# Optimization experiments

Hardware: AMD Instinct MI355X
Metric: run time of the kernel (lower is better)

The kernel has to match this reference:

```python
import jax, jax.numpy as jnp
import numpy as np
import math

DIM = 4096      # hidden size
NH = 32         # query heads
NKV = 8         # kv heads (GQA)
HD = 128        # head dim
SW = 4096       # sliding window / cache length
B = 8           # batch (decode)
START_POS = 2047
PAD_LEN = min(((START_POS + 1 + 31) // 32) * 32, SW)  # nearest_32 -> 2048
ROPE_THETA = 10000.0


def _rotation_matrix(pos, dhead, theta=ROPE_THETA):
    # freqs_to_rotation_matrix: block-diagonal 2x2 rotations, applied as q @ R
    freqs = 1.0 / (theta ** (np.arange(0, dhead, 2, dtype=np.float64) / dhead))
    ang = pos * freqs
    cos, sin = np.cos(ang), np.sin(ang)
    rot = np.zeros((dhead, dhead), dtype=np.float32)
    ev = np.arange(0, dhead, 2)
    od = ev + 1
    rot[ev, ev] = cos
    rot[od, od] = cos
    rot[ev, od] = -sin
    rot[od, ev] = sin
    return rot


def setup_inputs() -> dict:
    key = jax.random.key(0)
    ks = jax.random.split(key, 8)
    s = 0.02
    x = jax.random.normal(ks[0], (1, 1, B, DIM), jnp.float32)
    wq = jax.random.normal(ks[1], (DIM, NH * HD), jnp.float32) * s
    wk = jax.random.normal(ks[2], (DIM, NKV * HD), jnp.float32) * s
    wv = jax.random.normal(ks[3], (DIM, NKV * HD), jnp.float32) * s
    wo = jax.random.normal(ks[4], (NH * HD, DIM), jnp.float32) * s
    # true RoPE rotation matrix for the current position, same for all batch rows
    rot = jnp.asarray(_rotation_matrix(START_POS, HD))
    rot_mat = jnp.broadcast_to(rot, (1, B, HD, HD))
    # KV cache: valid history in [0, START_POS), rest is garbage that gets masked
    cache_k = jax.random.normal(ks[5], (B, NKV, SW, HD), jnp.float32) * s
    cache_v = jax.random.normal(ks[6], (B, NKV, SW, HD), jnp.float32) * s
    # additive mask: 0 for positions <= start_pos, finfo.min after
    neg = jnp.finfo(jnp.float32).min
    mask_row = jnp.where(jnp.arange(PAD_LEN) <= START_POS, 0.0, neg).astype(jnp.float32)
    attn_mask = jnp.broadcast_to(mask_row, (1, NH, B, PAD_LEN))
    return {
        "x": x, "wq": wq, "wk": wk, "wv": wv, "wo": wo,
        "rot_mat": rot_mat, "cache_k": cache_k, "cache_v": cache_v,
        "attn_mask": attn_mask, "start_pos": START_POS,
    }


def reference(x, wq, wk, wv, wo, rot_mat, cache_k, cache_v, attn_mask, start_pos):
    scale = 1.0 / math.sqrt(HD)
    xb = x[0, 0]                                  # (B, DIM)
    # fused QKV projection
    q = (xb @ wq).reshape(B, NH, HD)              # (B, NH, HD)
    k = (xb @ wk).reshape(B, NKV, HD)             # (B, NKV, HD)
    v = (xb @ wv).reshape(B, NKV, HD)             # (B, NKV, HD)
    # RoPE via explicit rotation-matrix matmul (per batch row)
    rm = rot_mat[0]                               # (B, HD, HD)
    q = jnp.einsum('bhd,bde->bhe', q, rm)
    k = jnp.einsum('bgd,bde->bge', k, rm)
    # update_cache at position `oldest` (= start_pos since start_pos < sliding_window)
    ck = cache_k.at[:, :, start_pos].set(k)
    cv = cache_v.at[:, :, start_pos].set(v)
    keys = ck[:, :, :PAD_LEN]                     # (B, NKV, L, HD)
    vals = cv[:, :, :PAD_LEN]                     # (B, NKV, L, HD)
    # grouped attention: NH query heads share NKV kv heads
    qg = q.reshape(B, NKV, NH // NKV, HD)
    scores = jnp.einsum('bgqd,bgld->bgql', qg, keys) * scale
    # attn_mask: (1, NH, B, L) -> (B, NKV, NH//NKV, L)
    mask = attn_mask[0].transpose(1, 0, 2).reshape(B, NKV, NH // NKV, PAD_LEN)
    probs = jax.nn.softmax(scores + mask, axis=-1)
    out = jnp.einsum('bgql,bgld->bgqd', probs, vals).reshape(B, NH * HD)
    dense = out @ wo                              # (B, DIM)
    return dense.reshape(1, 1, B, DIM)
```

## Files before the change

### kernel.cpp

```cpp
#include <hip/hip_runtime.h>
#include <math.h>

#define DIM 4096
#define NH 32
#define NKV 8
#define HD 128
#define B_ 8
#define SW 4096
#define PAD_LEN 2048
#define GQ 4
#define QKV_COLS (DIM + 2 * NKV * HD)
#define KSQ 64
#define KCQ (DIM / KSQ)
#define KSO 64
#define KCO (DIM / KSO)
#define LCHUNK 256
#define NLCHUNK (PAD_LEN / LCHUNK)
#define SCALE 0.08838834764831845f

#define OFF_QKVP   0
#define OFF_Q      (OFF_QKVP + KSQ * B_ * QKV_COLS)
#define OFF_K      (OFF_Q + B_ * DIM)
#define OFF_V      (OFF_K + B_ * NKV * HD)
#define OFF_AP     (OFF_V + B_ * NKV * HD)
#define OFF_AO     (OFF_AP + B_ * NKV * NLCHUNK * GQ * (HD + 2))
#define OFF_OP     (OFF_AO + B_ * DIM)

__global__ void qkv_partial(const float* __restrict__ x,
                            const float* __restrict__ wq,
                            const float* __restrict__ wk,
                            const float* __restrict__ wv,
                            float* __restrict__ part) {
    __shared__ float xs[B_][KCQ];
    const int tid = threadIdx.x;
    const int k0  = blockIdx.y * KCQ;

    {
        int idx = tid * 2;
        int r   = idx >> 6;
        int kk  = idx & (KCQ - 1);
        float2 xv = *(const float2*)(x + r * DIM + k0 + kk);
        xs[r][kk]     = xv.x;
        xs[r][kk + 1] = xv.y;
    }
    __syncthreads();

    const int bx = blockIdx.x;
    const float* W;
    int ldw, cbase;
    if (bx < 8)       { W = wq; ldw = NH * HD;  cbase = bx * 512; }
    else if (bx < 10) { W = wk; ldw = NKV * HD; cbase = (bx - 8) * 512; }
    else              { W = wv; ldw = NKV * HD; cbase = (bx - 10) * 512; }
    const int c = cbase + tid * 2;

    float2 acc[B_];
    #pragma unroll
    for (int r = 0; r < B_; ++r) { acc[r].x = 0.f; acc[r].y = 0.f; }

    const float* wp = W + (size_t)k0 * ldw + c;
    #pragma unroll 8
    for (int kk = 0; kk < KCQ; ++kk) {
        float2 w = *(const float2*)(wp + (size_t)kk * ldw);
        #pragma unroll
        for (int r = 0; r < B_; ++r) {
            float xv = xs[r][kk];
            acc[r].x = fmaf(xv, w.x, acc[r].x);
            acc[r].y = fmaf(xv, w.y, acc[r].y);
        }
    }
    const int colg = bx * 512 + tid * 2;
    #pragma unroll
    for (int r = 0; r < B_; ++r)
        *(float2*)(part + ((size_t)(blockIdx.y * B_ + r)) * QKV_COLS + colg) = acc[r];
}

__global__ void qkv_reduce_rope(const float* __restrict__ part,
                                const float* __restrict__ rot,
                                float* __restrict__ qb,
                                float* __restrict__ kb,
                                float* __restrict__ vb) {
    const int tid  = threadIdx.x;
    const int col2 = blockIdx.x * 256 + tid;
    const int col  = col2 * 2;
    const int r    = blockIdx.y;

    float2 v; v.x = 0.f; v.y = 0.f;
    #pragma unroll 8
    for (int s = 0; s < KSQ; ++s) {
        float2 p = *(const float2*)(part + ((size_t)(s * B_ + r)) * QKV_COLS + col);
        v.x += p.x; v.y += p.y;
    }

    if (col < DIM + NKV * HD) {
        int hd = col & (HD - 1);
        const float* rm = rot + (size_t)r * HD * HD;
        float c  = rm[hd * HD + hd];
        float sn = rm[(hd + 1) * HD + hd];
        float2 o;
        o.x = v.x * c + v.y * sn;
        o.y = v.y * c - v.x * sn;
        if (col < DIM) *(float2*)(qb + r * DIM + col) = o;
        else           *(float2*)(kb + r * NKV * HD + (col - DIM)) = o;
    } else {
        *(float2*)(vb + r * NKV * HD + (col - DIM - NKV * HD)) = v;
    }
}

__global__ void attn_partial(const float* __restrict__ qb,
                             const float* __restrict__ knew,
                             const float* __restrict__ vnew,
                             const float* __restrict__ cache_k,
                             const float* __restrict__ cache_v,
                             const float* __restrict__ mask,
                             const int* __restrict__ start_pos_p,
                             float* __restrict__ part) {
    const int bg = blockIdx.x;
    const int b  = bg >> 3;
    const int g  = bg & 7;
    const int chunk = blockIdx.y;
    const int l0 = chunk * LCHUNK;
    const int tid = threadIdx.x;
    const int sp = start_pos_p[0];

    __shared__ float q_lds[GQ][HD];
    __shared__ float p_lds[GQ][LCHUNK];
    __shared__ float crossm[4][GQ];
    __shared__ float crosss[4][GQ];

    for (int i = tid; i < GQ * HD; i += 256) {
        int qh = i >> 7;
        int d  = i & (HD - 1);
        q_lds[qh][d] = qb[b * DIM + (g * GQ + qh) * HD + d];
    }
    __syncthreads();

    const int l = l0 + tid;
    const float* krow = (l == sp) ? (knew + (b * NKV + g) * HD)
                                  : (cache_k + (((size_t)(b * NKV + g)) * SW + l) * HD);
    float s[GQ] = {0.f, 0.f, 0.f, 0.f};
    const float4* k4 = (const float4*)krow;
    #pragma unroll 8
    for (int j = 0; j < HD / 4; ++j) {
        float4 kv = k4[j];
        #pragma unroll
        for (int qh = 0; qh < GQ; ++qh) {
            s[qh] += kv.x * q_lds[qh][4*j]   + kv.y * q_lds[qh][4*j+1]
                   + kv.z * q_lds[qh][4*j+2] + kv.w * q_lds[qh][4*j+3];
        }
    }
    float sv[GQ];
    #pragma unroll
    for (int qh = 0; qh < GQ; ++qh)
        sv[qh] = s[qh] * SCALE
               + mask[(((size_t)(g * GQ + qh)) * B_ + b) * PAD_LEN + l];

    const int wave = tid >> 6;
    const int lane = tid & 63;
    float wm[GQ];
    #pragma unroll
    for (int qh = 0; qh < GQ; ++qh) wm[qh] = sv[qh];
    #pragma unroll
    for (int off = 32; off > 0; off >>= 1)
        #pragma unroll
        for (int qh = 0; qh < GQ; ++qh)
            wm[qh] = fmaxf(wm[qh], __shfl_xor(wm[qh], off, 64));
    if (lane == 0)
        #pragma unroll
        for (int qh = 0; qh < GQ; ++qh) crossm[wave][qh] = wm[qh];
    __syncthreads();
    float m[GQ];
    #pragma unroll
    for (int qh = 0; qh < GQ; ++qh)
        m[qh] = fmaxf(fmaxf(crossm[0][qh], crossm[1][qh]),
                      fmaxf(crossm[2][qh], crossm[3][qh]));

    float wsum[GQ];
    #pragma unroll
    for (int qh = 0; qh < GQ; ++qh) {
        float p = __expf(sv[qh] - m[qh]);
        p_lds[qh][tid] = p;
        wsum[qh] = p;
    }
    #pragma unroll
    for (int off = 32; off > 0; off >>= 1)
        #pragma unroll
        for (int qh = 0; qh < GQ; ++qh)
            wsum[qh] += __shfl_xor(wsum[qh], off, 64);
    if (lane == 0)
        #pragma unroll
        for (int qh = 0; qh < GQ; ++qh) crosss[wave][qh] = wsum[qh];
    __syncthreads();
    float sum[GQ];
    #pragma unroll
    for (int qh = 0; qh < GQ; ++qh)
        sum[qh] = crosss[0][qh] + crosss[1][qh] + crosss[2][qh] + crosss[3][qh];

    const int qh = wave;
    const int d2 = lane * 2;
    float2 acc; acc.x = 0.f; acc.y = 0.f;
    const float* vbase = cache_v + (((size_t)(b * NKV + g)) * SW) * HD + d2;
    const float* vnewp = vnew + (b * NKV + g) * HD + d2;
    #pragma unroll 4
    for (int ll = 0; ll < LCHUNK; ++ll) {
        int lg = l0 + ll;
        const float* vp = (lg == sp) ? vnewp : (vbase + (size_t)lg * HD);
        float2 vv = *(const float2*)vp;
        float p = p_lds[qh][ll];
        acc.x = fmaf(p, vv.x, acc.x);
        acc.y = fmaf(p, vv.y, acc.y);
    }

    const size_t base = ((size_t)bg * NLCHUNK + chunk) * GQ;
    *(float2*)(part + (base + qh) * (HD + 2) + 2 + d2) = acc;
    if (tid < GQ) {
        part[(base + tid) * (HD + 2) + 0] = m[tid];
        part[(base + tid) * (HD + 2) + 1] = sum[tid];
    }
}

__global__ void attn_combine(const float* __restrict__ part,
                             float* __restrict__ attnout) {
    const int bg = blockIdx.x;
    const int b  = bg >> 3;
    const int g  = bg & 7;
    const int d  = threadIdx.x;

    for (int qh = 0; qh < GQ; ++qh) {
        float M = -3.4e38f;
        #pragma unroll
        for (int c = 0; c < NLCHUNK; ++c)
            M = fmaxf(M, part[(((size_t)bg * NLCHUNK + c) * GQ + qh) * (HD + 2)]);
        float denom = 0.f, o = 0.f;
        #pragma unroll
        for (int c = 0; c < NLCHUNK; ++c) {
            const float* p = part + (((size_t)bg * NLCHUNK + c) * GQ + qh) * (HD + 2);
            float w = __expf(p[0] - M);
            denom += w * p[1];
            o     += w * p[2 + d];
        }
        attnout[b * DIM + (g * GQ + qh) * HD + d] = o / denom;
    }
}

__global__ void oproj_partial(const float* __restrict__ xin,
                              const float* __restrict__ wo,
                              float* __restrict__ part) {
    __shared__ float xs[B_][KCO];
    const int tid = threadIdx.x;
    const int k0  = blockIdx.y * KCO;

    {
        int idx = tid * 2;
        int r   = idx >> 6;
        int kk  = idx & (KCO - 1);
        float2 xv = *(const float2*)(xin + r * DIM + k0 + kk);
        xs[r][kk]     = xv.x;
        xs[r][kk + 1] = xv.y;
    }
    __syncthreads();

    const int col = blockIdx.x * 512 + tid * 2;
    float2 acc[B_];
    #pragma unroll
    for (int r = 0; r < B_; ++r) { acc[r].x = 0.f; acc[r].y = 0.f; }

    const float* wp = wo + (size_t)k0 * DIM + col;
    #pragma unroll 8
    for (int kk = 0; kk < KCO; ++kk) {
        float2 w = *(const float2*)(wp + (size_t)kk * DIM);
        #pragma unroll
        for (int r = 0; r < B_; ++r) {
            float xv = xs[r][kk];
            acc[r].x = fmaf(xv, w.x, acc[r].x);
            acc[r].y = fmaf(xv, w.y, acc[r].y);
        }
    }
    #pragma unroll
    for (int r = 0; r < B_; ++r)
        *(float2*)(part + ((size_t)(blockIdx.y * B_ + r)) * DIM + col) = acc[r];
}

__global__ void oproj_reduce(const float* __restrict__ part,
                             float* __restrict__ out) {
    const int tid = threadIdx.x;
    const int col = (blockIdx.x * 256 + tid) * 2;
    const int r   = blockIdx.y;
    float2 v; v.x = 0.f; v.y = 0.f;
    #pragma unroll 8
    for (int s = 0; s < KSO; ++s) {
        float2 p = *(const float2*)(part + ((size_t)(s * B_ + r)) * DIM + col);
        v.x += p.x; v.y += p.y;
    }
    *(float2*)(out + r * DIM + col) = v;
}

extern "C" void kernel_launch(void* const* d_in, const int* in_sizes, int n_in,
                              void* d_out, int out_size, void* d_ws, size_t ws_size,
                              hipStream_t stream) {
    const float* x        = (const float*)d_in[0];
    const float* wq       = (const float*)d_in[1];
    const float* wk       = (const float*)d_in[2];
    const float* wv       = (const float*)d_in[3];
    const float* wo       = (const float*)d_in[4];
    const float* rot      = (const float*)d_in[5];
    const float* cache_k  = (const float*)d_in[6];
    const float* cache_v  = (const float*)d_in[7];
    const float* mask     = (const float*)d_in[8];
    const int*   start_pp = (const int*)d_in[9];
    float* ws  = (float*)d_ws;
    float* out = (float*)d_out;

    dim3 gA(QKV_COLS / 512, KSQ);
    qkv_partial<<<gA, 256, 0, stream>>>(x, wq, wk, wv, ws + OFF_QKVP);

    dim3 gB((QKV_COLS / 2) / 256, B_);
    qkv_reduce_rope<<<gB, 256, 0, stream>>>(ws + OFF_QKVP, rot,
                                            ws + OFF_Q, ws + OFF_K, ws + OFF_V);

    dim3 gC(B_ * NKV, NLCHUNK);
    attn_partial<<<gC, 256, 0, stream>>>(ws + OFF_Q, ws + OFF_K, ws + OFF_V,
                                         cache_k, cache_v, mask, start_pp,
                                         ws + OFF_AP);

    attn_combine<<<dim3(B_ * NKV), 128, 0, stream>>>(ws + OFF_AP, ws + OFF_AO);

    dim3 gD(DIM / 512, KSO);
    oproj_partial<<<gD, 256, 0, stream>>>(ws + OFF_AO, wo, ws + OFF_OP);

    dim3 gE((DIM / 2) / 256, B_);
    oproj_reduce<<<gE, 256, 0, stream>>>(ws + OFF_OP, out);
}
```

Measured before the change: 129.3 us.

## Rework GEMV split-K with float4 tiles and restage attention via LDS

The QKV and output-projection GEMVs move to float4 column tiles with twice as many K-splits, and their reduce kernels split the partial sum across four waves and combine through shared memory. Attention uses 64-position chunks: each block stages K rows in padded shared memory, computes one query head per wave with a wave-local softmax, and accumulates V for all four heads before a cross-wave reduction. The goal is wider loads and more parallelism across the memory-bound stages. The cost is larger partial buffers, more combine work, and more blocks to schedule.

```diff
diff --git a/kernel.cpp b/kernel.cpp
--- a/kernel.cpp
+++ b/kernel.cpp
@@ -10,11 +10,11 @@
 #define PAD_LEN 2048
 #define GQ 4
 #define QKV_COLS (DIM + 2 * NKV * HD)
-#define KSQ 64
+#define KSQ 128
 #define KCQ (DIM / KSQ)
-#define KSO 64
+#define KSO 128
 #define KCO (DIM / KSO)
-#define LCHUNK 256
+#define LCHUNK 64
 #define NLCHUNK (PAD_LEN / LCHUNK)
 #define SCALE 0.08838834764831845f
 
@@ -26,200 +26,213 @@
 #define OFF_AO     (OFF_AP + B_ * NKV * NLCHUNK * GQ * (HD + 2))
 #define OFF_OP     (OFF_AO + B_ * DIM)
 
-__global__ void qkv_partial(const float* __restrict__ x,
-                            const float* __restrict__ wq,
-                            const float* __restrict__ wk,
-                            const float* __restrict__ wv,
-                            float* __restrict__ part) {
+__global__ __launch_bounds__(256)
+void qkv_partial(const float* __restrict__ x,
+                 const float* __restrict__ wq,
+                 const float* __restrict__ wk,
+                 const float* __restrict__ wv,
+                 float* __restrict__ part) {
     __shared__ float xs[B_][KCQ];
     const int tid = threadIdx.x;
     const int k0  = blockIdx.y * KCQ;
 
-    {
-        int idx = tid * 2;
-        int r   = idx >> 6;
-        int kk  = idx & (KCQ - 1);
-        float2 xv = *(const float2*)(x + r * DIM + k0 + kk);
-        xs[r][kk]     = xv.x;
-        xs[r][kk + 1] = xv.y;
+    if (tid < 64) {
+        int r  = tid >> 3;
+        int kk = (tid & 7) * 4;
+        *(float4*)&xs[r][kk] = *(const float4*)(x + r * DIM + k0 + kk);
     }
     __syncthreads();
 
     const int bx = blockIdx.x;
     const float* W;
     int ldw, cbase;
-    if (bx < 8)       { W = wq; ldw = NH * HD;  cbase = bx * 512; }
-    else if (bx < 10) { W = wk; ldw = NKV * HD; cbase = (bx - 8) * 512; }
-    else              { W = wv; ldw = NKV * HD; cbase = (bx - 10) * 512; }
-    const int c = cbase + tid * 2;
-
-    float2 acc[B_];
-    #pragma unroll
-    for (int r = 0; r < B_; ++r) { acc[r].x = 0.f; acc[r].y = 0.f; }
+    if (bx < 4)       { W = wq; ldw = NH * HD;  cbase = bx * 1024; }
+    else if (bx == 4) { W = wk; ldw = NKV * HD; cbase = 0; }
+    else              { W = wv; ldw = NKV * HD; cbase = 0; }
+    const int c = cbase + tid * 4;
+
+    float4 acc[B_];
+    #pragma unroll
+    for (int r = 0; r < B_; ++r) { acc[r].x = acc[r].y = acc[r].z = acc[r].w = 0.f; }
 
     const float* wp = W + (size_t)k0 * ldw + c;
     #pragma unroll 8
     for (int kk = 0; kk < KCQ; ++kk) {
-        float2 w = *(const float2*)(wp + (size_t)kk * ldw);
+        float4 w = *(const float4*)(wp + (size_t)kk * ldw);
         #pragma unroll
         for (int r = 0; r < B_; ++r) {
             float xv = xs[r][kk];
             acc[r].x = fmaf(xv, w.x, acc[r].x);
             acc[r].y = fmaf(xv, w.y, acc[r].y);
-        }
-    }
-    const int colg = bx * 512 + tid * 2;
+            acc[r].z = fmaf(xv, w.z, acc[r].z);
+            acc[r].w = fmaf(xv, w.w, acc[r].w);
+        }
+    }
+    const int colg = bx * 1024 + tid * 4;
     #pragma unroll
     for (int r = 0; r < B_; ++r)
-        *(float2*)(part + ((size_t)(blockIdx.y * B_ + r)) * QKV_COLS + colg) = acc[r];
-}
-
-__global__ void qkv_reduce_rope(const float* __restrict__ part,
-                                const float* __restrict__ rot,
-                                float* __restrict__ qb,
-                                float* __restrict__ kb,
-                                float* __restrict__ vb) {
-    const int tid  = threadIdx.x;
-    const int col2 = blockIdx.x * 256 + tid;
-    const int col  = col2 * 2;
+        *(float4*)(part + ((size_t)(blockIdx.y * B_ + r)) * QKV_COLS + colg) = acc[r];
+}
+
+__global__ __launch_bounds__(256)
+void qkv_reduce_rope(const float* __restrict__ part,
+                     const float* __restrict__ rot,
+                     float* __restrict__ qb,
+                     float* __restrict__ kb,
+                     float* __restrict__ vb) {
+    __shared__ float4 red[4][64];
+    const int tid = threadIdx.x;
+    const int sg  = tid >> 6;
+    const int c4l = tid & 63;
+    const int col4 = blockIdx.x * 64 + c4l;
     const int r    = blockIdx.y;
 
-    float2 v; v.x = 0.f; v.y = 0.f;
-    #pragma unroll 8
-    for (int s = 0; s < KSQ; ++s) {
-        float2 p = *(const float2*)(part + ((size_t)(s * B_ + r)) * QKV_COLS + col);
-        v.x += p.x; v.y += p.y;
-    }
-
-    if (col < DIM + NKV * HD) {
-        int hd = col & (HD - 1);
-        const float* rm = rot + (size_t)r * HD * HD;
-        float c  = rm[hd * HD + hd];
-        float sn = rm[(hd + 1) * HD + hd];
-        float2 o;
-        o.x = v.x * c + v.y * sn;
-        o.y = v.y * c - v.x * sn;
-        if (col < DIM) *(float2*)(qb + r * DIM + col) = o;
-        else           *(float2*)(kb + r * NKV * HD + (col - DIM)) = o;
-    } else {
-        *(float2*)(vb + r * NKV * HD + (col - DIM - NKV * HD)) = v;
-    }
-}
-
-__global__ void attn_partial(const float* __restrict__ qb,
-                             const float* __restrict__ knew,
-                             const float* __restrict__ vnew,
-                             const float* __restrict__ cache_k,
-                             const float* __restrict__ cache_v,
-                             const float* __restrict__ mask,
-                             const int* __restrict__ start_pos_p,
-                             float* __restrict__ part) {
+    float4 v; v.x = v.y = v.z = v.w = 0.f;
+    const int s0 = sg * (KSQ / 4);
+    #pragma unroll 8
+    for (int s = s0; s < s0 + KSQ / 4; ++s) {
+        float4 p = *(const float4*)(part + ((size_t)(s * B_ + r)) * QKV_COLS + col4 * 4);
+        v.x += p.x; v.y += p.y; v.z += p.z; v.w += p.w;
+    }
+    red[sg][c4l] = v;
+    __syncthreads();
+
+    if (tid < 64) {
+        const int c4 = blockIdx.x * 64 + tid;
+        float4 a = red[0][tid], b2 = red[1][tid], c2 = red[2][tid], d2 = red[3][tid];
+        float4 vv;
+        vv.x = a.x + b2.x + c2.x + d2.x;
+        vv.y = a.y + b2.y + c2.y + d2.y;
+        vv.z = a.z + b2.z + c2.z + d2.z;
+        vv.w = a.w + b2.w + c2.w + d2.w;
+        const int col = c4 * 4;
+        if (col < DIM + NKV * HD) {
+            int hd = col & (HD - 1);
+            const float* rm = rot + (size_t)r * HD * HD;
+            float c0 = rm[hd * HD + hd];
+            float s0r = rm[(hd + 1) * HD + hd];
+            float c1 = rm[(hd + 2) * HD + hd + 2];
+            float s1r = rm[(hd + 3) * HD + hd + 2];
+            float4 o;
+            o.x = vv.x * c0 + vv.y * s0r;
+            o.y = vv.y * c0 - vv.x * s0r;
+            o.z = vv.z * c1 + vv.w * s1r;
+            o.w = vv.w * c1 - vv.z * s1r;
+            if (col < DIM) *(float4*)(qb + r * DIM + col) = o;
+            else           *(float4*)(kb + r * NKV * HD + (col - DIM)) = o;
+        } else {
+            *(float4*)(vb + r * NKV * HD + (col - DIM - NKV * HD)) = vv;
+        }
+    }
+}
+
+__global__ __launch_bounds__(256)
+void attn_partial(const float* __restrict__ qb,
+                  const float* __restrict__ knew,
+                  const float* __restrict__ vnew,
+                  const float* __restrict__ cache_k,
+                  const float* __restrict__ cache_v,
+                  const float* __restrict__ mask,
+                  const int* __restrict__ start_pos_p,
+                  float* __restrict__ part) {
     const int bg = blockIdx.x;
     const int b  = bg >> 3;
     const int g  = bg & 7;
     const int chunk = blockIdx.y;
     const int l0 = chunk * LCHUNK;
-    const int tid = threadIdx.x;
+    const int tid  = threadIdx.x;
+    const int lane = tid & 63;
+    const int wave = tid >> 6;
     const int sp = start_pos_p[0];
 
+    __shared__ float k_lds[LCHUNK][HD + 4];
     __shared__ float q_lds[GQ][HD];
     __shared__ float p_lds[GQ][LCHUNK];
-    __shared__ float crossm[4][GQ];
-    __shared__ float crosss[4][GQ];
-
-    for (int i = tid; i < GQ * HD; i += 256) {
-        int qh = i >> 7;
-        int d  = i & (HD - 1);
-        q_lds[qh][d] = qb[b * DIM + (g * GQ + qh) * HD + d];
-    }
-    __syncthreads();
-
-    const int l = l0 + tid;
-    const float* krow = (l == sp) ? (knew + (b * NKV + g) * HD)
-                                  : (cache_k + (((size_t)(b * NKV + g)) * SW + l) * HD);
-    float s[GQ] = {0.f, 0.f, 0.f, 0.f};
-    const float4* k4 = (const float4*)krow;
-    #pragma unroll 8
-    for (int j = 0; j < HD / 4; ++j) {
-        float4 kv = k4[j];
+    __shared__ float vred[4][GQ][HD];
+
+    if (tid < 128) {
+        int qh = tid >> 5;
+        int d4 = (tid & 31) * 4;
+        *(float4*)&q_lds[qh][d4] = *(const float4*)(qb + b * DIM + (g * GQ + qh) * HD + d4);
+    }
+    const float* kc = cache_k + ((size_t)(b * NKV + g)) * SW * HD;
+    const float* knp = knew + (b * NKV + g) * HD;
+    #pragma unroll
+    for (int i = 0; i < 8; ++i) {
+        int idx = i * 256 + tid;
+        int r   = idx >> 5;
+        int c4  = (idx & 31) * 4;
+        int lg  = l0 + r;
+        const float* src = (lg == sp) ? knp : (kc + (size_t)lg * HD);
+        *(float4*)&k_lds[r][c4] = *(const float4*)(src + c4);
+    }
+    __syncthreads();
+
+    const int qh = wave;
+    const int row = lane;
+    float s = 0.f;
+    #pragma unroll 8
+    for (int d = 0; d < HD; d += 4) {
+        float4 kv = *(const float4*)&k_lds[row][d];
+        float4 qv = *(const float4*)&q_lds[qh][d];
+        s += kv.x * qv.x + kv.y * qv.y + kv.z * qv.z + kv.w * qv.w;
+    }
+    const int l = l0 + row;
+    float sv = s * SCALE + mask[(((size_t)(g * GQ + qh)) * B_ + b) * PAD_LEN + l];
+
+    float m = sv;
+    #pragma unroll
+    for (int off = 32; off > 0; off >>= 1)
+        m = fmaxf(m, __shfl_xor(m, off, 64));
+    float p = __expf(sv - m);
+    float sum = p;
+    #pragma unroll
+    for (int off = 32; off > 0; off >>= 1)
+        sum += __shfl_xor(sum, off, 64);
+    p_lds[qh][row] = p;
+    __syncthreads();
+
+    const int d2 = lane * 2;
+    const float* vc  = cache_v + ((size_t)(b * NKV + g)) * SW * HD;
+    const float* vnp = vnew + (b * NKV + g) * HD;
+    float2 acc[GQ];
+    #pragma unroll
+    for (int q = 0; q < GQ; ++q) { acc[q].x = 0.f; acc[q].y = 0.f; }
+    #pragma unroll 4
+    for (int ll = 0; ll < LCHUNK / 4; ++ll) {
+        int r  = wave * (LCHUNK / 4) + ll;
+        int lg = l0 + r;
+        const float* vp = ((lg == sp) ? vnp : (vc + (size_t)lg * HD)) + d2;
+        float2 vv = *(const float2*)vp;
         #pragma unroll
-        for (int qh = 0; qh < GQ; ++qh) {
-            s[qh] += kv.x * q_lds[qh][4*j]   + kv.y * q_lds[qh][4*j+1]
-                   + kv.z * q_lds[qh][4*j+2] + kv.w * q_lds[qh][4*j+3];
-        }
-    }
-    float sv[GQ];
-    #pragma unroll
-    for (int qh = 0; qh < GQ; ++qh)
-        sv[qh] = s[qh] * SCALE
-               + mask[(((size_t)(g * GQ + qh)) * B_ + b) * PAD_LEN + l];
-
-    const int wave = tid >> 6;
-    const int lane = tid & 63;
-    float wm[GQ];
-    #pragma unroll
-    for (int qh = 0; qh < GQ; ++qh) wm[qh] = sv[qh];
-    #pragma unroll
-    for (int off = 32; off > 0; off >>= 1)
-        #pragma unroll
-        for (int qh = 0; qh < GQ; ++qh)
-            wm[qh] = fmaxf(wm[qh], __shfl_xor(wm[qh], off, 64));
-    if (lane == 0)
-        #pragma unroll
-        for (int qh = 0; qh < GQ; ++qh) crossm[wave][qh] = wm[qh];
-    __syncthreads();
-    float m[GQ];
-    #pragma unroll
-    for (int qh = 0; qh < GQ; ++qh)
-        m[qh] = fmaxf(fmaxf(crossm[0][qh], crossm[1][qh]),
-                      fmaxf(crossm[2][qh], crossm[3][qh]));
-
-    float wsum[GQ];
-    #pragma unroll
-    for (int qh = 0; qh < GQ; ++qh) {
-        float p = __expf(sv[qh] - m[qh]);
-        p_lds[qh][tid] = p;
-        wsum[qh] = p;
-    }
-    #pragma unroll
-    for (int off = 32; off > 0; off >>= 1)
-        #pragma unroll
-        for (int qh = 0; qh < GQ; ++qh)
-            wsum[qh] += __shfl_xor(wsum[qh], off, 64);
-    if (lane == 0)
-        #pragma unroll
-        for (int qh = 0; qh < GQ; ++qh) crosss[wave][qh] = wsum[qh];
-    __syncthreads();
-    float sum[GQ];
-    #pragma unroll
-    for (int qh = 0; qh < GQ; ++qh)
-        sum[qh] = crosss[0][qh] + crosss[1][qh] + crosss[2][qh] + crosss[3][qh];
-
-    const int qh = wave;
-    const int d2 = lane * 2;
-    float2 acc; acc.x = 0.f; acc.y = 0.f;
-    const float* vbase = cache_v + (((size_t)(b * NKV + g)) * SW) * HD + d2;
-    const float* vnewp = vnew + (b * NKV + g) * HD + d2;
-    #pragma unroll 4
-    for (int ll = 0; ll < LCHUNK; ++ll) {
-        int lg = l0 + ll;
-        const float* vp = (lg == sp) ? vnewp : (vbase + (size_t)lg * HD);
-        float2 vv = *(const float2*)vp;
-        float p = p_lds[qh][ll];
-        acc.x = fmaf(p, vv.x, acc.x);
-        acc.y = fmaf(p, vv.y, acc.y);
-    }
-
+        for (int q = 0; q < GQ; ++q) {
+            float pp = p_lds[q][r];
+            acc[q].x = fmaf(pp, vv.x, acc[q].x);
+            acc[q].y = fmaf(pp, vv.y, acc[q].y);
+        }
+    }
+    #pragma unroll
+    for (int q = 0; q < GQ; ++q)
+        *(float2*)&vred[wave][q][d2] = acc[q];
+    __syncthreads();
+
+    float2 o; o.x = 0.f; o.y = 0.f;
+    #pragma unroll
+    for (int w = 0; w < 4; ++w) {
+        float2 t = *(const float2*)&vred[w][qh][d2];
+        o.x += t.x; o.y += t.y;
+    }
     const size_t base = ((size_t)bg * NLCHUNK + chunk) * GQ;
-    *(float2*)(part + (base + qh) * (HD + 2) + 2 + d2) = acc;
-    if (tid < GQ) {
-        part[(base + tid) * (HD + 2) + 0] = m[tid];
-        part[(base + tid) * (HD + 2) + 1] = sum[tid];
-    }
-}
-
-__global__ void attn_combine(const float* __restrict__ part,
-                             float* __restrict__ attnout) {
+    *(float2*)(part + (base + qh) * (HD + 2) + 2 + d2) = o;
+    if (lane == 0) {
+        part[(base + qh) * (HD + 2) + 0] = m;
+        part[(base + qh) * (HD + 2) + 1] = sum;
+    }
+}
+
+__global__ __launch_bounds__(128)
+void attn_combine(const float* __restrict__ part,
+                  float* __restrict__ attnout) {
     const int bg = blockIdx.x;
     const int b  = bg >> 3;
     const int g  = bg & 7;
@@ -227,11 +240,11 @@
 
     for (int qh = 0; qh < GQ; ++qh) {
         float M = -3.4e38f;
-        #pragma unroll
+        #pragma unroll 8
         for (int c = 0; c < NLCHUNK; ++c)
             M = fmaxf(M, part[(((size_t)bg * NLCHUNK + c) * GQ + qh) * (HD + 2)]);
         float denom = 0.f, o = 0.f;
-        #pragma unroll
+        #pragma unroll 8
         for (int c = 0; c < NLCHUNK; ++c) {
             const float* p = part + (((size_t)bg * NLCHUNK + c) * GQ + qh) * (HD + 2);
             float w = __expf(p[0] - M);
@@ -242,56 +255,74 @@
     }
 }
 
-__global__ void oproj_partial(const float* __restrict__ xin,
-                              const float* __restrict__ wo,
-                              float* __restrict__ part) {
+__global__ __launch_bounds__(256)
+void oproj_partial(const float* __restrict__ xin,
+                   const float* __restrict__ wo,
+                   float* __restrict__ part) {
     __shared__ float xs[B_][KCO];
     const int tid = threadIdx.x;
     const int k0  = blockIdx.y * KCO;
 
-    {
-        int idx = tid * 2;
-        int r   = idx >> 6;
-        int kk  = idx & (KCO - 1);
-        float2 xv = *(const float2*)(xin + r * DIM + k0 + kk);
-        xs[r][kk]     = xv.x;
-        xs[r][kk + 1] = xv.y;
-    }
-    __syncthreads();
-
-    const int col = blockIdx.x * 512 + tid * 2;
-    float2 acc[B_];
-    #pragma unroll
-    for (int r = 0; r < B_; ++r) { acc[r].x = 0.f; acc[r].y = 0.f; }
+    if (tid < 64) {
+        int r  = tid >> 3;
+        int kk = (tid & 7) * 4;
+        *(float4*)&xs[r][kk] = *(const float4*)(xin + r * DIM + k0 + kk);
+    }
+    __syncthreads();
+
+    const int col = blockIdx.x * 1024 + tid * 4;
+    float4 acc[B_];
+    #pragma unroll
+    for (int r = 0; r < B_; ++r) { acc[r].x = acc[r].y = acc[r].z = acc[r].w = 0.f; }
 
     const float* wp = wo + (size_t)k0 * DIM + col;
     #pragma unroll 8
     for (int kk = 0; kk < KCO; ++kk) {
-        float2 w = *(const float2*)(wp + (size_t)kk * DIM);
+        float4 w = *(const float4*)(wp + (size_t)kk * DIM);
         #pragma unroll
         for (int r = 0; r < B_; ++r) {
             float xv = xs[r][kk];
             acc[r].x = fmaf(xv, w.x, acc[r].x);
             acc[r].y = fmaf(xv, w.y, acc[r].y);
+            acc[r].z = fmaf(xv, w.z, acc[r].z);
+            acc[r].w = fmaf(xv, w.w, acc[r].w);
         }
     }
     #pragma unroll
     for (int r = 0; r < B_; ++r)
-        *(float2*)(part + ((size_t)(blockIdx.y * B_ + r)) * DIM + col) = acc[r];
-}
-
-__global__ void oproj_reduce(const float* __restrict__ part,
-                             float* __restrict__ out) {
+        *(float4*)(part + ((size_t)(blockIdx.y * B_ + r)) * DIM + col) = acc[r];
+}
+
+__global__ __launch_bounds__(256)
+void oproj_reduce(const float* __restrict__ part,
+                  float* __restrict__ out) {
+    __shared__ float4 red[4][64];
     const int tid = threadIdx.x;
-    const int col = (blockIdx.x * 256 + tid) * 2;
-    const int r   = blockIdx.y;
-    float2 v; v.x = 0.f; v.y = 0.f;
-    #pragma unroll 8
-    for (int s = 0; s < KSO; ++s) {
-        float2 p = *(const float2*)(part + ((size_t)(s * B_ + r)) * DIM + col);
-        v.x += p.x; v.y += p.y;
-    }
-    *(float2*)(out + r * DIM + col) = v;
+    const int sg  = tid >> 6;
+    const int c4l = tid & 63;
+    const int col4 = blockIdx.x * 64 + c4l;
+    const int r    = blockIdx.y;
+
+    float4 v; v.x = v.y = v.z = v.w = 0.f;
+    const int s0 = sg * (KSO / 4);
+    #pragma unroll 8
+    for (int s = s0; s < s0 + KSO / 4; ++s) {
+        float4 p = *(const float4*)(part + ((size_t)(s * B_ + r)) * DIM + col4 * 4);
+        v.x += p.x; v.y += p.y; v.z += p.z; v.w += p.w;
+    }
+    red[sg][c4l] = v;
+    __syncthreads();
+
+    if (tid < 64) {
+        const int c4 = blockIdx.x * 64 + tid;
+        float4 a = red[0][tid], b2 = red[1][tid], c2 = red[2][tid], d2 = red[3][tid];
+        float4 o;
+        o.x = a.x + b2.x + c2.x + d2.x;
+        o.y = a.y + b2.y + c2.y + d2.y;
+        o.z = a.z + b2.z + c2.z + d2.z;
+        o.w = a.w + b2.w + c2.w + d2.w;
+        *(float4*)(out + r * DIM + c4 * 4) = o;
+    }
 }
 
 extern "C" void kernel_launch(void* const* d_in, const int* in_sizes, int n_in,
@@ -310,10 +341,10 @@
     float* ws  = (float*)d_ws;
     float* out = (float*)d_out;
 
-    dim3 gA(QKV_COLS / 512, KSQ);
+    dim3 gA(6, KSQ);
     qkv_partial<<<gA, 256, 0, stream>>>(x, wq, wk, wv, ws + OFF_QKVP);
 
-    dim3 gB((QKV_COLS / 2) / 256, B_);
+    dim3 gB(QKV_COLS / 256, B_);
     qkv_reduce_rope<<<gB, 256, 0, stream>>>(ws + OFF_QKVP, rot,
                                             ws + OFF_Q, ws + OFF_K, ws + OFF_V);
 
@@ -324,9 +355,9 @@
 
     attn_combine<<<dim3(B_ * NKV), 128, 0, stream>>>(ws + OFF_AP, ws + OFF_AO);
 
-    dim3 gD(DIM / 512, KSO);
+    dim3 gD(4, KSO);
     oproj_partial<<<gD, 256, 0, stream>>>(ws + OFF_AO, wo, ws + OFF_OP);
 
-    dim3 gE((DIM / 2) / 256, B_);
+    dim3 gE(DIM / 256, B_);
     oproj_reduce<<<gE, 256, 0, stream>>>(ws + OFF_OP, out);
 }
```

New measurement: 115.9 us. 10.4% less time.
